# Performance work log

Hardware: AMD Instinct MI355X
Metric: run time of the kernel (lower is better)

The kernel has to match this reference:

```python
import jax, jax.numpy as jnp
import numpy as np

N_ATOMS = 768
BOX_L = 30.0
CUTOFF = 5.0


def _cp(a, b, c):
    # numpy equivalent of torch.cartesian_prod for 1-D inputs
    g = np.meshgrid(a, b, c, indexing='ij')
    return np.stack(g, axis=-1).reshape(-1, 3)


def get_shifts_np(box, pbc, cutoff):
    # host-side mirror of TorchNeighborList._get_shifts (data-dependent shapes)
    recip = np.linalg.inv(box).T
    inv_len = np.linalg.norm(recip, axis=1)
    nrep = np.where(pbc, np.ceil(cutoff * inv_len).astype(np.int64), 0)
    r1 = np.arange(1, nrep[0] + 1)
    r2 = np.arange(1, nrep[1] + 1)
    r3 = np.arange(1, nrep[2] + 1)
    o = np.zeros(1, dtype=np.int64)
    blocks = [_cp(r1, r2, r3), _cp(r1, r2, o), _cp(r1, r2, -r3),
              _cp(r1, o, r3), _cp(r1, o, o), _cp(r1, o, -r3),
              _cp(r1, -r2, r3), _cp(r1, -r2, o), _cp(r1, -r2, -r3),
              _cp(o, r2, r3), _cp(o, r2, o), _cp(o, r2, -r3), _cp(o, o, r3)]
    return np.concatenate(blocks, axis=0).astype(np.int32)


def setup_inputs() -> dict:
    key = jax.random.key(0)
    positions = jax.random.uniform(key, (N_ATOMS, 3), dtype=jnp.float32) * BOX_L
    box = jnp.eye(3, dtype=jnp.float32) * BOX_L
    shifts = jnp.asarray(get_shifts_np(np.eye(3) * BOX_L, np.array([True, True, True]), CUTOFF))  # (13, 3)
    return {"positions": positions, "box": box, "shifts": shifts, "cutoff": CUTOFF}


def reference(positions, box, shifts, cutoff):
    N = positions.shape[0]
    S = shifts.shape[0]
    # central-cell unique pairs i<j (torch.combinations)
    iu, ju = jnp.triu_indices(N, k=1)
    # shifted candidates: cartesian_prod(shift_index, i, j)
    shift_idx = jnp.repeat(jnp.arange(S), N * N)
    pi_s = jnp.tile(jnp.repeat(jnp.arange(N), N), S)
    pj_s = jnp.tile(jnp.arange(N), S * N)
    pi_all = jnp.concatenate([iu, pi_s])          # (P,)
    pj_all = jnp.concatenate([ju, pj_s])          # (P,)
    shifts_all = jnp.concatenate([jnp.zeros((iu.shape[0], 3), dtype=shifts.dtype), shifts[shift_idx]])  # (P,3)
    shift_vals = shifts_all.astype(box.dtype) @ box
    Rij = positions[pi_all] - positions[pj_all] + shift_vals  # (P,3)
    d = jnp.linalg.norm(Rij, axis=1)
    mask = d < cutoff
    # bidirectional pairs (torch.cat of (i,j) and (j,i)), offsets negated for the first half
    bi_i = jnp.concatenate([pi_all, pj_all])
    bi_j = jnp.concatenate([pj_all, pi_all])
    bi_off = jnp.concatenate([-shifts_all, shifts_all])
    bi_mask = jnp.concatenate([mask, mask])
    # jit-compatible compaction: sort by idx_i with invalid entries pushed to the end
    sort_key = jnp.where(bi_mask, bi_i, N)
    order = jnp.argsort(sort_key)  # jax sort is stable
    valid = bi_mask[order]
    idx_i = jnp.where(valid, bi_i[order], -1)
    idx_j = jnp.where(valid, bi_j[order], -1)
    offset = (bi_off[order].astype(box.dtype) @ box) * valid[:, None].astype(box.dtype)
    return idx_i, idx_j, offset, valid
```

## Files before the change

### kernel.cpp

```cpp
#include <hip/hip_runtime.h>

#pragma clang fp contract(off)


#define MAX_SHIFTS 64
#define FILL_ITERS 16

typedef float f32x4 __attribute__((ext_vector_type(4)));

__device__ __forceinline__ bool pv_fwd(float fx, float fy, float fz,
                                       const float* __restrict__ pos, int j,
                                       float sx, float sy, float sz, float cutoff) {
  float dx = fx - pos[j * 3 + 0] + sx;
  float dy = fy - pos[j * 3 + 1] + sy;
  float dz = fz - pos[j * 3 + 2] + sz;
  float d2 = dx * dx + dy * dy + dz * dz;
  return sqrtf(d2) < cutoff;
}

__device__ __forceinline__ bool pv_bwd(const float* __restrict__ pos, int a,
                                       float fx, float fy, float fz,
                                       float sx, float sy, float sz, float cutoff) {
  float dx = pos[a * 3 + 0] - fx + sx;
  float dy = pos[a * 3 + 1] - fy + sy;
  float dz = pos[a * 3 + 2] - fz + sz;
  float d2 = dx * dx + dy * dy + dz * dz;
  return sqrtf(d2) < cutoff;
}

__device__ __forceinline__ void load_shift_vecs(const float* __restrict__ box,
                                                const int* __restrict__ shifts,
                                                int S, float* sv, int tid, int nthreads) {
  for (int s = tid; s < S; s += nthreads) {
    float s0 = (float)shifts[s * 3 + 0];
    float s1 = (float)shifts[s * 3 + 1];
    float s2 = (float)shifts[s * 3 + 2];
    sv[s * 3 + 0] = s0 * box[0] + s1 * box[3] + s2 * box[6];
    sv[s * 3 + 1] = s0 * box[1] + s1 * box[4] + s2 * box[7];
    sv[s * 3 + 2] = s0 * box[2] + s1 * box[5] + s2 * box[8];
  }
}

__device__ __forceinline__ bool axis_ok(float lo, float hi, float cutpad) {
  return (hi > -cutpad) && (lo < cutpad);
}

__global__ __launch_bounds__(256) void k_count(
    const float* __restrict__ pos, const float* __restrict__ box,
    const int* __restrict__ shifts, const float* __restrict__ cutp,
    int N, int S, int* __restrict__ count) {
  __shared__ float sv[MAX_SHIFTS * 3];
  __shared__ float bred[4][6];
  __shared__ int rf[4], rb[4];
  int atom = blockIdx.x;
  int t = threadIdx.x;
  float cut = cutp[0];
  float cutpad = cut + fmaxf(cut * 1e-5f, 1e-5f);
  load_shift_vecs(box, shifts, S, sv, t, blockDim.x);

  float mnx = 1e30f, mny = 1e30f, mnz = 1e30f, mxx = -1e30f, mxy = -1e30f, mxz = -1e30f;
  for (int i = t; i < N; i += blockDim.x) {
    float x = pos[3 * i + 0], y = pos[3 * i + 1], z = pos[3 * i + 2];
    mnx = fminf(mnx, x); mny = fminf(mny, y); mnz = fminf(mnz, z);
    mxx = fmaxf(mxx, x); mxy = fmaxf(mxy, y); mxz = fmaxf(mxz, z);
  }
  for (int off = 32; off; off >>= 1) {
    mnx = fminf(mnx, __shfl_xor(mnx, off)); mny = fminf(mny, __shfl_xor(mny, off));
    mnz = fminf(mnz, __shfl_xor(mnz, off)); mxx = fmaxf(mxx, __shfl_xor(mxx, off));
    mxy = fmaxf(mxy, __shfl_xor(mxy, off)); mxz = fmaxf(mxz, __shfl_xor(mxz, off));
  }
  int w = t >> 6;
  if ((t & 63) == 0) {
    bred[w][0] = mnx; bred[w][1] = mny; bred[w][2] = mnz;
    bred[w][3] = mxx; bred[w][4] = mxy; bred[w][5] = mxz;
  }
  __syncthreads();
  int nw = blockDim.x >> 6;
  mnx = bred[0][0]; mny = bred[0][1]; mnz = bred[0][2];
  mxx = bred[0][3]; mxy = bred[0][4]; mxz = bred[0][5];
  for (int ww = 1; ww < nw; ww++) {
    mnx = fminf(mnx, bred[ww][0]); mny = fminf(mny, bred[ww][1]); mnz = fminf(mnz, bred[ww][2]);
    mxx = fmaxf(mxx, bred[ww][3]); mxy = fmaxf(mxy, bred[ww][4]); mxz = fmaxf(mxz, bred[ww][5]);
  }

  float pix = pos[3 * atom + 0], piy = pos[3 * atom + 1], piz = pos[3 * atom + 2];
  int cf = 0, cb = 0;
  for (int j = atom + 1 + t; j < N; j += blockDim.x)
    if (pv_fwd(pix, piy, piz, pos, j, 0.f, 0.f, 0.f, cut)) cf++;
  for (int a = t; a < atom; a += blockDim.x)
    if (pv_bwd(pos, a, pix, piy, piz, 0.f, 0.f, 0.f, cut)) cb++;

  for (int s = 0; s < S; s++) {
    float svx = sv[3 * s + 0], svy = sv[3 * s + 1], svz = sv[3 * s + 2];
    bool af = axis_ok((pix - mxx) + svx, (pix - mnx) + svx, cutpad) &&
              axis_ok((piy - mxy) + svy, (piy - mny) + svy, cutpad) &&
              axis_ok((piz - mxz) + svz, (piz - mnz) + svz, cutpad);
    if (af) {
      for (int j = t; j < N; j += blockDim.x)
        if (pv_fwd(pix, piy, piz, pos, j, svx, svy, svz, cut)) cf++;
    }
    bool ab = axis_ok((mnx - pix) + svx, (mxx - pix) + svx, cutpad) &&
              axis_ok((mny - piy) + svy, (mxy - piy) + svy, cutpad) &&
              axis_ok((mnz - piz) + svz, (mxz - piz) + svz, cutpad);
    if (ab) {
      for (int a = t; a < N; a += blockDim.x)
        if (pv_bwd(pos, a, pix, piy, piz, svx, svy, svz, cut)) cb++;
    }
  }
  for (int off = 32; off; off >>= 1) {
    cf += __shfl_down(cf, off);
    cb += __shfl_down(cb, off);
  }
  if ((t & 63) == 0) { rf[w] = cf; rb[w] = cb; }
  __syncthreads();
  if (t == 0) {
    int f = 0, b = 0;
    for (int ww = 0; ww < nw; ww++) { f += rf[ww]; b += rb[ww]; }
    count[2 * atom + 0] = f;
    count[2 * atom + 1] = b;
  }
}

__global__ __launch_bounds__(256) void k_main(
    const float* __restrict__ pos, const float* __restrict__ box,
    const int* __restrict__ shifts, const float* __restrict__ cutp,
    int N, int S, const int* __restrict__ count,
    float* __restrict__ out, long M, long n4, int NWB) {
  __shared__ float sv[MAX_SHIFTS * 3];
  int t = threadIdx.x;
  int lane = t & 63, w = t >> 6;
  int n2 = 2 * N;

  if ((int)blockIdx.x < NWB) {
    float cut = cutp[0];
    float cutpad = cut + fmaxf(cut * 1e-5f, 1e-5f);
    load_shift_vecs(box, shifts, S, sv, t, 256);
    __syncthreads();
    int g = blockIdx.x * 4 + w;
    if (g >= n2) return;
    int atom = g >> 1;
    int dir = g & 1;

    float mnx = 1e30f, mny = 1e30f, mnz = 1e30f, mxx = -1e30f, mxy = -1e30f, mxz = -1e30f;
    for (int i = lane; i < N; i += 64) {
      float x = pos[3 * i + 0], y = pos[3 * i + 1], z = pos[3 * i + 2];
      mnx = fminf(mnx, x); mny = fminf(mny, y); mnz = fminf(mnz, z);
      mxx = fmaxf(mxx, x); mxy = fmaxf(mxy, y); mxz = fmaxf(mxz, z);
    }
    for (int off = 32; off; off >>= 1) {
      mnx = fminf(mnx, __shfl_xor(mnx, off)); mny = fminf(mny, __shfl_xor(mny, off));
      mnz = fminf(mnz, __shfl_xor(mnz, off)); mxx = fmaxf(mxx, __shfl_xor(mxx, off));
      mxy = fmaxf(mxy, __shfl_xor(mxy, off)); mxz = fmaxf(mxz, __shfl_xor(mxz, off));
    }

    int pre = 0;
    for (int i = lane; i < g; i += 64) pre += count[i];
    for (int off = 32; off; off >>= 1) pre += __shfl_xor(pre, off);
    long base = pre;

    float* __restrict__ out_i = out;
    float* __restrict__ out_j = out + M;
    float* __restrict__ out_off = out + 2 * M;
    float* __restrict__ out_v = out + 5 * M;

    float pix = pos[3 * atom + 0], piy = pos[3 * atom + 1], piz = pos[3 * atom + 2];
    float fatom = (float)atom;
    int running = 0;

    {
      int n = (dir == 0) ? (N - 1 - atom) : atom;
      int j0 = (dir == 0) ? (atom + 1) : 0;
      float oz0 = (dir == 0) ? -0.0f : 0.0f;
      for (int c0 = 0; c0 < n; c0 += 64) {
        int c = c0 + lane;
        bool v = false;
        int other = j0 + c;
        if (c < n) {
          v = (dir == 0) ? pv_fwd(pix, piy, piz, pos, other, 0.f, 0.f, 0.f, cut)
                         : pv_bwd(pos, other, pix, piy, piz, 0.f, 0.f, 0.f, cut);
        }
        unsigned long long m = __ballot(v);
        if (v) {
          int rank = __popcll(m & ((1ULL << lane) - 1ULL));
          long row = base + running + rank;
          out_i[row] = fatom;
          out_j[row] = (float)other;
          out_off[row * 3 + 0] = oz0;
          out_off[row * 3 + 1] = oz0;
          out_off[row * 3 + 2] = oz0;
          out_v[row] = 1.0f;
        }
        running += __popcll(m);
      }
    }
    for (int s = 0; s < S; s++) {
      float svx = sv[3 * s + 0], svy = sv[3 * s + 1], svz = sv[3 * s + 2];
      bool active;
      if (dir == 0) {
        active = axis_ok((pix - mxx) + svx, (pix - mnx) + svx, cutpad) &&
                 axis_ok((piy - mxy) + svy, (piy - mny) + svy, cutpad) &&
                 axis_ok((piz - mxz) + svz, (piz - mnz) + svz, cutpad);
      } else {
        active = axis_ok((mnx - pix) + svx, (mxx - pix) + svx, cutpad) &&
                 axis_ok((mny - piy) + svy, (mxy - piy) + svy, cutpad) &&
                 axis_ok((mnz - piz) + svz, (mxz - piz) + svz, cutpad);
      }
      if (!active) continue;
      float ox = (dir == 0) ? -svx : svx;
      float oy = (dir == 0) ? -svy : svy;
      float oz = (dir == 0) ? -svz : svz;
      for (int c0 = 0; c0 < N; c0 += 64) {
        int other = c0 + lane;
        bool v = false;
        if (other < N) {
          v = (dir == 0) ? pv_fwd(pix, piy, piz, pos, other, svx, svy, svz, cut)
                         : pv_bwd(pos, other, pix, piy, piz, svx, svy, svz, cut);
        }
        unsigned long long m = __ballot(v);
        if (v) {
          int rank = __popcll(m & ((1ULL << lane) - 1ULL));
          long row = base + running + rank;
          out_i[row] = fatom;
          out_j[row] = (float)other;
          out_off[row * 3 + 0] = ox;
          out_off[row * 3 + 1] = oy;
          out_off[row * 3 + 2] = oz;
          out_v[row] = 1.0f;
        }
        running += __popcll(m);
      }
    }
  } else {
    int tot = 0;
    for (int i = lane; i < n2; i += 64) tot += count[i];
    for (int off = 32; off; off >>= 1) tot += __shfl_xor(tot, off);
    long total = tot;

    long fb = (long)blockIdx.x - NWB;
    long k_lo = fb * (256L * FILL_ITERS);
    long k_hi = k_lo + 256L * FILL_ITERS;
    if (k_hi > n4) k_hi = n4;
    long e_lo = k_lo << 2, e_hi = k_hi << 2;

    long E0 = total;
    long E1 = M + total;
    long E2 = 2 * M + 3 * total;
    long E3 = 5 * M + total;
    const f32x4 neg = {-1.f, -1.f, -1.f, -1.f};
    const f32x4 zer = {0.f, 0.f, 0.f, 0.f};
    f32x4* __restrict__ out4 = (f32x4*)out;

    int s0 = (e_lo < M) ? 0 : ((e_lo < 2 * M) ? 1 : ((e_lo < 5 * M) ? 2 : 3));
    long eh = e_hi - 1;
    int s1 = (eh < M) ? 0 : ((eh < 2 * M) ? 1 : ((eh < 5 * M) ? 2 : 3));
    long ve0 = (s0 == 0) ? E0 : ((s0 == 1) ? E1 : ((s0 == 2) ? E2 : E3));

    if ((k_hi - k_lo) == 256L * FILL_ITERS && s0 == s1 && e_lo >= ve0) {
      f32x4 val = (s0 < 2) ? neg : zer;
      f32x4* __restrict__ p = out4 + k_lo + t;
#pragma unroll
      for (int it = 0; it < FILL_ITERS; it++) p[(long)it * 256] = val;
    } else {
      for (int it = 0; it < FILL_ITERS; it++) {
        long k = k_lo + (long)it * 256 + t;
        if (k >= n4) break;
        long e = k << 2;
        long ve = (e < M) ? E0 : ((e < 2 * M) ? E1 : ((e < 5 * M) ? E2 : E3));
        if (e + 4 <= ve) continue;
        bool isneg = (e < 2 * M);
        if (e >= ve) {
          out4[k] = isneg ? neg : zer;
        } else {
          float dv = isneg ? -1.f : 0.f;
          for (int q = 0; q < 4; q++)
            if (e + q >= ve) out[e + q] = dv;
        }
      }
    }
  }
}

extern "C" void kernel_launch(void* const* d_in, const int* in_sizes, int n_in,
                              void* d_out, int out_size, void* d_ws, size_t ws_size,
                              hipStream_t stream) {
  const float* pos = (const float*)d_in[0];
  const float* box = (const float*)d_in[1];
  const int* shifts = (const int*)d_in[2];
  const float* cutp = (const float*)d_in[3];
  int N = in_sizes[0] / 3;
  int S = in_sizes[2] / 3;
  long M = (long)out_size / 6;
  float* out = (float*)d_out;

  int* count = (int*)d_ws;

  long n4 = (long)out_size / 4;
  int NWB = (2 * N + 3) / 4;
  int NFB = (int)((n4 + (256L * FILL_ITERS) - 1) / (256L * FILL_ITERS));

  hipLaunchKernelGGL(k_count, dim3(N), dim3(256), 0, stream,
                     pos, box, shifts, cutp, N, S, count);
  hipLaunchKernelGGL(k_main, dim3(NWB + NFB), dim3(256), 0, stream,
                     pos, box, shifts, cutp, N, S, count, out, M, n4, NWB);
}
```

Measured before the change: 94.28 us.

## Fuse count and write kernels into persistent kernel with grid barrier

Merges the counting kernel and the main write/fill kernel into one persistent kernel launched with a fixed grid of 256 blocks. Blocks loop over atoms, then meet at a global atomic barrier, then loop over write groups and fill chunks. This removes one kernel launch and the per-warp recomputation of the bounding box, but adds a memset, a spin-wait barrier, and less parallelism in the count phase (256 blocks instead of N). The barrier depends on every block being resident at the same time, which launch_bounds(256,2) is meant to ensure.

```diff
diff --git a/kernel.cpp b/kernel.cpp
--- a/kernel.cpp
+++ b/kernel.cpp
@@ -5,6 +5,7 @@
 
 #define MAX_SHIFTS 64
 #define FILL_ITERS 16
+#define NBLK 256
 
 typedef float f32x4 __attribute__((ext_vector_type(4)));
 
@@ -28,10 +29,25 @@
   return sqrtf(d2) < cutoff;
 }
 
-__device__ __forceinline__ void load_shift_vecs(const float* __restrict__ box,
-                                                const int* __restrict__ shifts,
-                                                int S, float* sv, int tid, int nthreads) {
-  for (int s = tid; s < S; s += nthreads) {
+__device__ __forceinline__ bool axis_ok(float lo, float hi, float cutpad) {
+  return (hi > -cutpad) && (lo < cutpad);
+}
+
+__global__ __launch_bounds__(256, 2) void k_fused(
+    const float* __restrict__ pos, const float* __restrict__ box,
+    const int* __restrict__ shifts, const float* __restrict__ cutp,
+    int N, int S, int* bar, int* count,
+    float* __restrict__ out, long M, long n4, int NWB, int C) {
+  __shared__ float sv[MAX_SHIFTS * 3];
+  __shared__ float bred[4][6];
+  __shared__ int rf[4], rb[4];
+  int t = threadIdx.x;
+  int lane = t & 63, w = t >> 6;
+  int n2 = 2 * N;
+  float cut = cutp[0];
+  float cutpad = cut + fmaxf(cut * 1e-5f, 1e-5f);
+
+  for (int s = t; s < S; s += 256) {
     float s0 = (float)shifts[s * 3 + 0];
     float s1 = (float)shifts[s * 3 + 1];
     float s2 = (float)shifts[s * 3 + 2];
@@ -39,27 +55,9 @@
     sv[s * 3 + 1] = s0 * box[1] + s1 * box[4] + s2 * box[7];
     sv[s * 3 + 2] = s0 * box[2] + s1 * box[5] + s2 * box[8];
   }
-}
-
-__device__ __forceinline__ bool axis_ok(float lo, float hi, float cutpad) {
-  return (hi > -cutpad) && (lo < cutpad);
-}
-
-__global__ __launch_bounds__(256) void k_count(
-    const float* __restrict__ pos, const float* __restrict__ box,
-    const int* __restrict__ shifts, const float* __restrict__ cutp,
-    int N, int S, int* __restrict__ count) {
-  __shared__ float sv[MAX_SHIFTS * 3];
-  __shared__ float bred[4][6];
-  __shared__ int rf[4], rb[4];
-  int atom = blockIdx.x;
-  int t = threadIdx.x;
-  float cut = cutp[0];
-  float cutpad = cut + fmaxf(cut * 1e-5f, 1e-5f);
-  load_shift_vecs(box, shifts, S, sv, t, blockDim.x);
 
   float mnx = 1e30f, mny = 1e30f, mnz = 1e30f, mxx = -1e30f, mxy = -1e30f, mxz = -1e30f;
-  for (int i = t; i < N; i += blockDim.x) {
+  for (int i = t; i < N; i += 256) {
     float x = pos[3 * i + 0], y = pos[3 * i + 1], z = pos[3 * i + 2];
     mnx = fminf(mnx, x); mny = fminf(mny, y); mnz = fminf(mnz, z);
     mxx = fmaxf(mxx, x); mxy = fmaxf(mxy, y); mxz = fmaxf(mxz, z);
@@ -69,99 +67,82 @@
     mnz = fminf(mnz, __shfl_xor(mnz, off)); mxx = fmaxf(mxx, __shfl_xor(mxx, off));
     mxy = fmaxf(mxy, __shfl_xor(mxy, off)); mxz = fmaxf(mxz, __shfl_xor(mxz, off));
   }
-  int w = t >> 6;
   if ((t & 63) == 0) {
     bred[w][0] = mnx; bred[w][1] = mny; bred[w][2] = mnz;
     bred[w][3] = mxx; bred[w][4] = mxy; bred[w][5] = mxz;
   }
   __syncthreads();
-  int nw = blockDim.x >> 6;
   mnx = bred[0][0]; mny = bred[0][1]; mnz = bred[0][2];
   mxx = bred[0][3]; mxy = bred[0][4]; mxz = bred[0][5];
-  for (int ww = 1; ww < nw; ww++) {
+  for (int ww = 1; ww < 4; ww++) {
     mnx = fminf(mnx, bred[ww][0]); mny = fminf(mny, bred[ww][1]); mnz = fminf(mnz, bred[ww][2]);
     mxx = fmaxf(mxx, bred[ww][3]); mxy = fmaxf(mxy, bred[ww][4]); mxz = fmaxf(mxz, bred[ww][5]);
   }
 
-  float pix = pos[3 * atom + 0], piy = pos[3 * atom + 1], piz = pos[3 * atom + 2];
-  int cf = 0, cb = 0;
-  for (int j = atom + 1 + t; j < N; j += blockDim.x)
-    if (pv_fwd(pix, piy, piz, pos, j, 0.f, 0.f, 0.f, cut)) cf++;
-  for (int a = t; a < atom; a += blockDim.x)
-    if (pv_bwd(pos, a, pix, piy, piz, 0.f, 0.f, 0.f, cut)) cb++;
-
-  for (int s = 0; s < S; s++) {
-    float svx = sv[3 * s + 0], svy = sv[3 * s + 1], svz = sv[3 * s + 2];
-    bool af = axis_ok((pix - mxx) + svx, (pix - mnx) + svx, cutpad) &&
-              axis_ok((piy - mxy) + svy, (piy - mny) + svy, cutpad) &&
-              axis_ok((piz - mxz) + svz, (piz - mnz) + svz, cutpad);
-    if (af) {
-      for (int j = t; j < N; j += blockDim.x)
-        if (pv_fwd(pix, piy, piz, pos, j, svx, svy, svz, cut)) cf++;
-    }
-    bool ab = axis_ok((mnx - pix) + svx, (mxx - pix) + svx, cutpad) &&
-              axis_ok((mny - piy) + svy, (mxy - piy) + svy, cutpad) &&
-              axis_ok((mnz - piz) + svz, (mxz - piz) + svz, cutpad);
-    if (ab) {
-      for (int a = t; a < N; a += blockDim.x)
-        if (pv_bwd(pos, a, pix, piy, piz, svx, svy, svz, cut)) cb++;
-    }
-  }
-  for (int off = 32; off; off >>= 1) {
-    cf += __shfl_down(cf, off);
-    cb += __shfl_down(cb, off);
-  }
-  if ((t & 63) == 0) { rf[w] = cf; rb[w] = cb; }
+  for (int atom = blockIdx.x; atom < N; atom += gridDim.x) {
+    float pix = pos[3 * atom + 0], piy = pos[3 * atom + 1], piz = pos[3 * atom + 2];
+    int cf = 0, cb = 0;
+    for (int j = atom + 1 + t; j < N; j += 256)
+      if (pv_fwd(pix, piy, piz, pos, j, 0.f, 0.f, 0.f, cut)) cf++;
+    for (int a = t; a < atom; a += 256)
+      if (pv_bwd(pos, a, pix, piy, piz, 0.f, 0.f, 0.f, cut)) cb++;
+
+    for (int s = 0; s < S; s++) {
+      float svx = sv[3 * s + 0], svy = sv[3 * s + 1], svz = sv[3 * s + 2];
+      bool af = axis_ok((pix - mxx) + svx, (pix - mnx) + svx, cutpad) &&
+                axis_ok((piy - mxy) + svy, (piy - mny) + svy, cutpad) &&
+                axis_ok((piz - mxz) + svz, (piz - mnz) + svz, cutpad);
+      if (af) {
+        for (int j = t; j < N; j += 256)
+          if (pv_fwd(pix, piy, piz, pos, j, svx, svy, svz, cut)) cf++;
+      }
+      bool ab = axis_ok((mnx - pix) + svx, (mxx - pix) + svx, cutpad) &&
+                axis_ok((mny - piy) + svy, (mxy - piy) + svy, cutpad) &&
+                axis_ok((mnz - piz) + svz, (mxz - piz) + svz, cutpad);
+      if (ab) {
+        for (int a = t; a < N; a += 256)
+          if (pv_bwd(pos, a, pix, piy, piz, svx, svy, svz, cut)) cb++;
+      }
+    }
+    for (int off = 32; off; off >>= 1) {
+      cf += __shfl_down(cf, off);
+      cb += __shfl_down(cb, off);
+    }
+    if ((t & 63) == 0) { rf[w] = cf; rb[w] = cb; }
+    __syncthreads();
+    if (t == 0) {
+      count[2 * atom + 0] = rf[0] + rf[1] + rf[2] + rf[3];
+      count[2 * atom + 1] = rb[0] + rb[1] + rb[2] + rb[3];
+    }
+    __syncthreads();
+  }
+
   __syncthreads();
   if (t == 0) {
-    int f = 0, b = 0;
-    for (int ww = 0; ww < nw; ww++) { f += rf[ww]; b += rb[ww]; }
-    count[2 * atom + 0] = f;
-    count[2 * atom + 1] = b;
-  }
-}
-
-__global__ __launch_bounds__(256) void k_main(
-    const float* __restrict__ pos, const float* __restrict__ box,
-    const int* __restrict__ shifts, const float* __restrict__ cutp,
-    int N, int S, const int* __restrict__ count,
-    float* __restrict__ out, long M, long n4, int NWB) {
-  __shared__ float sv[MAX_SHIFTS * 3];
-  int t = threadIdx.x;
-  int lane = t & 63, w = t >> 6;
-  int n2 = 2 * N;
-
-  if ((int)blockIdx.x < NWB) {
-    float cut = cutp[0];
-    float cutpad = cut + fmaxf(cut * 1e-5f, 1e-5f);
-    load_shift_vecs(box, shifts, S, sv, t, 256);
-    __syncthreads();
-    int g = blockIdx.x * 4 + w;
-    if (g >= n2) return;
+    __hip_atomic_fetch_add(bar, 1, __ATOMIC_ACQ_REL, __HIP_MEMORY_SCOPE_AGENT);
+    while (__hip_atomic_load(bar, __ATOMIC_ACQUIRE, __HIP_MEMORY_SCOPE_AGENT) <
+           (int)gridDim.x) {
+      __builtin_amdgcn_s_sleep(2);
+    }
+  }
+  __syncthreads();
+
+  float* __restrict__ out_i = out;
+  float* __restrict__ out_j = out + M;
+  float* __restrict__ out_off = out + 2 * M;
+  float* __restrict__ out_v = out + 5 * M;
+
+  for (int wb = blockIdx.x; wb < NWB; wb += gridDim.x) {
+    int g = wb * 4 + w;
+    if (g >= n2) continue;
     int atom = g >> 1;
     int dir = g & 1;
 
-    float mnx = 1e30f, mny = 1e30f, mnz = 1e30f, mxx = -1e30f, mxy = -1e30f, mxz = -1e30f;
-    for (int i = lane; i < N; i += 64) {
-      float x = pos[3 * i + 0], y = pos[3 * i + 1], z = pos[3 * i + 2];
-      mnx = fminf(mnx, x); mny = fminf(mny, y); mnz = fminf(mnz, z);
-      mxx = fmaxf(mxx, x); mxy = fmaxf(mxy, y); mxz = fmaxf(mxz, z);
-    }
-    for (int off = 32; off; off >>= 1) {
-      mnx = fminf(mnx, __shfl_xor(mnx, off)); mny = fminf(mny, __shfl_xor(mny, off));
-      mnz = fminf(mnz, __shfl_xor(mnz, off)); mxx = fmaxf(mxx, __shfl_xor(mxx, off));
-      mxy = fmaxf(mxy, __shfl_xor(mxy, off)); mxz = fmaxf(mxz, __shfl_xor(mxz, off));
-    }
-
     int pre = 0;
-    for (int i = lane; i < g; i += 64) pre += count[i];
+    for (int i = lane; i < g; i += 64)
+      pre += __hip_atomic_load(&count[i], __ATOMIC_RELAXED, __HIP_MEMORY_SCOPE_AGENT);
     for (int off = 32; off; off >>= 1) pre += __shfl_xor(pre, off);
     long base = pre;
-
-    float* __restrict__ out_i = out;
-    float* __restrict__ out_j = out + M;
-    float* __restrict__ out_off = out + 2 * M;
-    float* __restrict__ out_v = out + 5 * M;
 
     float pix = pos[3 * atom + 0], piy = pos[3 * atom + 1], piz = pos[3 * atom + 2];
     float fatom = (float)atom;
@@ -230,25 +211,27 @@
         running += __popcll(m);
       }
     }
-  } else {
-    int tot = 0;
-    for (int i = lane; i < n2; i += 64) tot += count[i];
-    for (int off = 32; off; off >>= 1) tot += __shfl_xor(tot, off);
-    long total = tot;
-
-    long fb = (long)blockIdx.x - NWB;
-    long k_lo = fb * (256L * FILL_ITERS);
+  }
+
+  int tot = 0;
+  for (int i = lane; i < n2; i += 64)
+    tot += __hip_atomic_load(&count[i], __ATOMIC_RELAXED, __HIP_MEMORY_SCOPE_AGENT);
+  for (int off = 32; off; off >>= 1) tot += __shfl_xor(tot, off);
+  long total = tot;
+
+  long E0 = total;
+  long E1 = M + total;
+  long E2 = 2 * M + 3 * total;
+  long E3 = 5 * M + total;
+  const f32x4 neg = {-1.f, -1.f, -1.f, -1.f};
+  const f32x4 zer = {0.f, 0.f, 0.f, 0.f};
+  f32x4* __restrict__ out4 = (f32x4*)out;
+
+  for (int chunk = blockIdx.x; chunk < C; chunk += gridDim.x) {
+    long k_lo = (long)chunk * (256L * FILL_ITERS);
     long k_hi = k_lo + 256L * FILL_ITERS;
     if (k_hi > n4) k_hi = n4;
     long e_lo = k_lo << 2, e_hi = k_hi << 2;
-
-    long E0 = total;
-    long E1 = M + total;
-    long E2 = 2 * M + 3 * total;
-    long E3 = 5 * M + total;
-    const f32x4 neg = {-1.f, -1.f, -1.f, -1.f};
-    const f32x4 zer = {0.f, 0.f, 0.f, 0.f};
-    f32x4* __restrict__ out4 = (f32x4*)out;
 
     int s0 = (e_lo < M) ? 0 : ((e_lo < 2 * M) ? 1 : ((e_lo < 5 * M) ? 2 : 3));
     long eh = e_hi - 1;
@@ -292,14 +275,15 @@
   long M = (long)out_size / 6;
   float* out = (float*)d_out;
 
-  int* count = (int*)d_ws;
+  int* bar = (int*)d_ws;
+  int* count = (int*)d_ws + 4;
 
   long n4 = (long)out_size / 4;
   int NWB = (2 * N + 3) / 4;
-  int NFB = (int)((n4 + (256L * FILL_ITERS) - 1) / (256L * FILL_ITERS));
-
-  hipLaunchKernelGGL(k_count, dim3(N), dim3(256), 0, stream,
-                     pos, box, shifts, cutp, N, S, count);
-  hipLaunchKernelGGL(k_main, dim3(NWB + NFB), dim3(256), 0, stream,
-                     pos, box, shifts, cutp, N, S, count, out, M, n4, NWB);
-}
+  int C = (int)((n4 + (256L * FILL_ITERS) - 1) / (256L * FILL_ITERS));
+
+  hipMemsetAsync(bar, 0, sizeof(int), stream);
+  hipLaunchKernelGGL(k_fused, dim3(NBLK), dim3(256), 0, stream,
+                     pos, box, shifts, cutp, N, S, bar, count,
+                     out, M, n4, NWB, C);
+}
```

Result: slower. 139.3 us (+47.7%).

## Move padding fill into count kernel, overlapping it with pair counting

Applied to the files above, without the earlier changes.

The full-buffer fill of padding values (-1 for indices, 0 for offsets and valid) moves from the second kernel into the first one. It runs as extra blocks beside the per-atom counting blocks, and the scatter kernel later overwrites the valid rows. The fill no longer has to wait for the counts and skips the per-element boundary logic, so the output write traffic overlaps with counting. The cost is that the whole buffer is written, including rows the scatter then rewrites, which adds some redundant write bandwidth.

```diff
diff --git a/kernel.cpp b/kernel.cpp
--- a/kernel.cpp
+++ b/kernel.cpp
@@ -28,10 +28,47 @@
   return sqrtf(d2) < cutoff;
 }
 
-__device__ __forceinline__ void load_shift_vecs(const float* __restrict__ box,
-                                                const int* __restrict__ shifts,
-                                                int S, float* sv, int tid, int nthreads) {
-  for (int s = tid; s < S; s += nthreads) {
+__device__ __forceinline__ bool axis_ok(float lo, float hi, float cutpad) {
+  return (hi > -cutpad) && (lo < cutpad);
+}
+
+__global__ __launch_bounds__(256) void k_phase1(
+    const float* __restrict__ pos, const float* __restrict__ box,
+    const int* __restrict__ shifts, const float* __restrict__ cutp,
+    int N, int S, int* __restrict__ count,
+    float* __restrict__ out, long M, long n4, int NFB) {
+  int t = threadIdx.x;
+
+  if ((int)blockIdx.x < NFB) {
+    long k_lo = (long)blockIdx.x * (256L * FILL_ITERS);
+    long k_hi = k_lo + 256L * FILL_ITERS;
+    if (k_hi > n4) k_hi = n4;
+    long m4 = (2 * M) >> 2;
+    const f32x4 neg = {-1.f, -1.f, -1.f, -1.f};
+    const f32x4 zer = {0.f, 0.f, 0.f, 0.f};
+    f32x4* __restrict__ out4 = (f32x4*)out;
+
+    if (k_hi - k_lo == 256L * FILL_ITERS && (k_hi <= m4 || k_lo >= m4)) {
+      f32x4 val = (k_lo < m4) ? neg : zer;
+      f32x4* __restrict__ p = out4 + k_lo + t;
+#pragma unroll
+      for (int it = 0; it < FILL_ITERS; it++) p[(long)it * 256] = val;
+    } else {
+      for (long k = k_lo + t; k < k_hi; k += 256)
+        out4[k] = (k < m4) ? neg : zer;
+    }
+    return;
+  }
+
+  __shared__ float sv[MAX_SHIFTS * 3];
+  __shared__ float bred[4][6];
+  __shared__ int rf[4], rb[4];
+  int atom = (int)blockIdx.x - NFB;
+  int w = t >> 6;
+  float cut = cutp[0];
+  float cutpad = cut + fmaxf(cut * 1e-5f, 1e-5f);
+
+  for (int s = t; s < S; s += 256) {
     float s0 = (float)shifts[s * 3 + 0];
     float s1 = (float)shifts[s * 3 + 1];
     float s2 = (float)shifts[s * 3 + 2];
@@ -39,27 +76,9 @@
     sv[s * 3 + 1] = s0 * box[1] + s1 * box[4] + s2 * box[7];
     sv[s * 3 + 2] = s0 * box[2] + s1 * box[5] + s2 * box[8];
   }
-}
-
-__device__ __forceinline__ bool axis_ok(float lo, float hi, float cutpad) {
-  return (hi > -cutpad) && (lo < cutpad);
-}
-
-__global__ __launch_bounds__(256) void k_count(
-    const float* __restrict__ pos, const float* __restrict__ box,
-    const int* __restrict__ shifts, const float* __restrict__ cutp,
-    int N, int S, int* __restrict__ count) {
-  __shared__ float sv[MAX_SHIFTS * 3];
-  __shared__ float bred[4][6];
-  __shared__ int rf[4], rb[4];
-  int atom = blockIdx.x;
-  int t = threadIdx.x;
-  float cut = cutp[0];
-  float cutpad = cut + fmaxf(cut * 1e-5f, 1e-5f);
-  load_shift_vecs(box, shifts, S, sv, t, blockDim.x);
 
   float mnx = 1e30f, mny = 1e30f, mnz = 1e30f, mxx = -1e30f, mxy = -1e30f, mxz = -1e30f;
-  for (int i = t; i < N; i += blockDim.x) {
+  for (int i = t; i < N; i += 256) {
     float x = pos[3 * i + 0], y = pos[3 * i + 1], z = pos[3 * i + 2];
     mnx = fminf(mnx, x); mny = fminf(mny, y); mnz = fminf(mnz, z);
     mxx = fmaxf(mxx, x); mxy = fmaxf(mxy, y); mxz = fmaxf(mxz, z);
@@ -69,25 +88,23 @@
     mnz = fminf(mnz, __shfl_xor(mnz, off)); mxx = fmaxf(mxx, __shfl_xor(mxx, off));
     mxy = fmaxf(mxy, __shfl_xor(mxy, off)); mxz = fmaxf(mxz, __shfl_xor(mxz, off));
   }
-  int w = t >> 6;
   if ((t & 63) == 0) {
     bred[w][0] = mnx; bred[w][1] = mny; bred[w][2] = mnz;
     bred[w][3] = mxx; bred[w][4] = mxy; bred[w][5] = mxz;
   }
   __syncthreads();
-  int nw = blockDim.x >> 6;
   mnx = bred[0][0]; mny = bred[0][1]; mnz = bred[0][2];
   mxx = bred[0][3]; mxy = bred[0][4]; mxz = bred[0][5];
-  for (int ww = 1; ww < nw; ww++) {
+  for (int ww = 1; ww < 4; ww++) {
     mnx = fminf(mnx, bred[ww][0]); mny = fminf(mny, bred[ww][1]); mnz = fminf(mnz, bred[ww][2]);
     mxx = fmaxf(mxx, bred[ww][3]); mxy = fmaxf(mxy, bred[ww][4]); mxz = fmaxf(mxz, bred[ww][5]);
   }
 
   float pix = pos[3 * atom + 0], piy = pos[3 * atom + 1], piz = pos[3 * atom + 2];
   int cf = 0, cb = 0;
-  for (int j = atom + 1 + t; j < N; j += blockDim.x)
+  for (int j = atom + 1 + t; j < N; j += 256)
     if (pv_fwd(pix, piy, piz, pos, j, 0.f, 0.f, 0.f, cut)) cf++;
-  for (int a = t; a < atom; a += blockDim.x)
+  for (int a = t; a < atom; a += 256)
     if (pv_bwd(pos, a, pix, piy, piz, 0.f, 0.f, 0.f, cut)) cb++;
 
   for (int s = 0; s < S; s++) {
@@ -96,14 +113,14 @@
               axis_ok((piy - mxy) + svy, (piy - mny) + svy, cutpad) &&
               axis_ok((piz - mxz) + svz, (piz - mnz) + svz, cutpad);
     if (af) {
-      for (int j = t; j < N; j += blockDim.x)
+      for (int j = t; j < N; j += 256)
         if (pv_fwd(pix, piy, piz, pos, j, svx, svy, svz, cut)) cf++;
     }
     bool ab = axis_ok((mnx - pix) + svx, (mxx - pix) + svx, cutpad) &&
               axis_ok((mny - piy) + svy, (mxy - piy) + svy, cutpad) &&
               axis_ok((mnz - piz) + svz, (mxz - piz) + svz, cutpad);
     if (ab) {
-      for (int a = t; a < N; a += blockDim.x)
+      for (int a = t; a < N; a += 256)
         if (pv_bwd(pos, a, pix, piy, piz, svx, svy, svz, cut)) cb++;
     }
   }
@@ -114,168 +131,125 @@
   if ((t & 63) == 0) { rf[w] = cf; rb[w] = cb; }
   __syncthreads();
   if (t == 0) {
-    int f = 0, b = 0;
-    for (int ww = 0; ww < nw; ww++) { f += rf[ww]; b += rb[ww]; }
-    count[2 * atom + 0] = f;
-    count[2 * atom + 1] = b;
-  }
-}
-
-__global__ __launch_bounds__(256) void k_main(
+    count[2 * atom + 0] = rf[0] + rf[1] + rf[2] + rf[3];
+    count[2 * atom + 1] = rb[0] + rb[1] + rb[2] + rb[3];
+  }
+}
+
+__global__ __launch_bounds__(256) void k_rows(
     const float* __restrict__ pos, const float* __restrict__ box,
     const int* __restrict__ shifts, const float* __restrict__ cutp,
     int N, int S, const int* __restrict__ count,
-    float* __restrict__ out, long M, long n4, int NWB) {
+    float* __restrict__ out, long M) {
   __shared__ float sv[MAX_SHIFTS * 3];
   int t = threadIdx.x;
   int lane = t & 63, w = t >> 6;
   int n2 = 2 * N;
-
-  if ((int)blockIdx.x < NWB) {
-    float cut = cutp[0];
-    float cutpad = cut + fmaxf(cut * 1e-5f, 1e-5f);
-    load_shift_vecs(box, shifts, S, sv, t, 256);
-    __syncthreads();
-    int g = blockIdx.x * 4 + w;
-    if (g >= n2) return;
-    int atom = g >> 1;
-    int dir = g & 1;
-
-    float mnx = 1e30f, mny = 1e30f, mnz = 1e30f, mxx = -1e30f, mxy = -1e30f, mxz = -1e30f;
-    for (int i = lane; i < N; i += 64) {
-      float x = pos[3 * i + 0], y = pos[3 * i + 1], z = pos[3 * i + 2];
-      mnx = fminf(mnx, x); mny = fminf(mny, y); mnz = fminf(mnz, z);
-      mxx = fmaxf(mxx, x); mxy = fmaxf(mxy, y); mxz = fmaxf(mxz, z);
-    }
-    for (int off = 32; off; off >>= 1) {
-      mnx = fminf(mnx, __shfl_xor(mnx, off)); mny = fminf(mny, __shfl_xor(mny, off));
-      mnz = fminf(mnz, __shfl_xor(mnz, off)); mxx = fmaxf(mxx, __shfl_xor(mxx, off));
-      mxy = fmaxf(mxy, __shfl_xor(mxy, off)); mxz = fmaxf(mxz, __shfl_xor(mxz, off));
-    }
-
-    int pre = 0;
-    for (int i = lane; i < g; i += 64) pre += count[i];
-    for (int off = 32; off; off >>= 1) pre += __shfl_xor(pre, off);
-    long base = pre;
-
-    float* __restrict__ out_i = out;
-    float* __restrict__ out_j = out + M;
-    float* __restrict__ out_off = out + 2 * M;
-    float* __restrict__ out_v = out + 5 * M;
-
-    float pix = pos[3 * atom + 0], piy = pos[3 * atom + 1], piz = pos[3 * atom + 2];
-    float fatom = (float)atom;
-    int running = 0;
-
-    {
-      int n = (dir == 0) ? (N - 1 - atom) : atom;
-      int j0 = (dir == 0) ? (atom + 1) : 0;
-      float oz0 = (dir == 0) ? -0.0f : 0.0f;
-      for (int c0 = 0; c0 < n; c0 += 64) {
-        int c = c0 + lane;
-        bool v = false;
-        int other = j0 + c;
-        if (c < n) {
-          v = (dir == 0) ? pv_fwd(pix, piy, piz, pos, other, 0.f, 0.f, 0.f, cut)
-                         : pv_bwd(pos, other, pix, piy, piz, 0.f, 0.f, 0.f, cut);
-        }
-        unsigned long long m = __ballot(v);
-        if (v) {
-          int rank = __popcll(m & ((1ULL << lane) - 1ULL));
-          long row = base + running + rank;
-          out_i[row] = fatom;
-          out_j[row] = (float)other;
-          out_off[row * 3 + 0] = oz0;
-          out_off[row * 3 + 1] = oz0;
-          out_off[row * 3 + 2] = oz0;
-          out_v[row] = 1.0f;
-        }
-        running += __popcll(m);
-      }
-    }
-    for (int s = 0; s < S; s++) {
-      float svx = sv[3 * s + 0], svy = sv[3 * s + 1], svz = sv[3 * s + 2];
-      bool active;
-      if (dir == 0) {
-        active = axis_ok((pix - mxx) + svx, (pix - mnx) + svx, cutpad) &&
-                 axis_ok((piy - mxy) + svy, (piy - mny) + svy, cutpad) &&
-                 axis_ok((piz - mxz) + svz, (piz - mnz) + svz, cutpad);
-      } else {
-        active = axis_ok((mnx - pix) + svx, (mxx - pix) + svx, cutpad) &&
-                 axis_ok((mny - piy) + svy, (mxy - piy) + svy, cutpad) &&
-                 axis_ok((mnz - piz) + svz, (mxz - piz) + svz, cutpad);
-      }
-      if (!active) continue;
-      float ox = (dir == 0) ? -svx : svx;
-      float oy = (dir == 0) ? -svy : svy;
-      float oz = (dir == 0) ? -svz : svz;
-      for (int c0 = 0; c0 < N; c0 += 64) {
-        int other = c0 + lane;
-        bool v = false;
-        if (other < N) {
-          v = (dir == 0) ? pv_fwd(pix, piy, piz, pos, other, svx, svy, svz, cut)
-                         : pv_bwd(pos, other, pix, piy, piz, svx, svy, svz, cut);
-        }
-        unsigned long long m = __ballot(v);
-        if (v) {
-          int rank = __popcll(m & ((1ULL << lane) - 1ULL));
-          long row = base + running + rank;
-          out_i[row] = fatom;
-          out_j[row] = (float)other;
-          out_off[row * 3 + 0] = ox;
-          out_off[row * 3 + 1] = oy;
-          out_off[row * 3 + 2] = oz;
-          out_v[row] = 1.0f;
-        }
-        running += __popcll(m);
-      }
-    }
-  } else {
-    int tot = 0;
-    for (int i = lane; i < n2; i += 64) tot += count[i];
-    for (int off = 32; off; off >>= 1) tot += __shfl_xor(tot, off);
-    long total = tot;
-
-    long fb = (long)blockIdx.x - NWB;
-    long k_lo = fb * (256L * FILL_ITERS);
-    long k_hi = k_lo + 256L * FILL_ITERS;
-    if (k_hi > n4) k_hi = n4;
-    long e_lo = k_lo << 2, e_hi = k_hi << 2;
-
-    long E0 = total;
-    long E1 = M + total;
-    long E2 = 2 * M + 3 * total;
-    long E3 = 5 * M + total;
-    const f32x4 neg = {-1.f, -1.f, -1.f, -1.f};
-    const f32x4 zer = {0.f, 0.f, 0.f, 0.f};
-    f32x4* __restrict__ out4 = (f32x4*)out;
-
-    int s0 = (e_lo < M) ? 0 : ((e_lo < 2 * M) ? 1 : ((e_lo < 5 * M) ? 2 : 3));
-    long eh = e_hi - 1;
-    int s1 = (eh < M) ? 0 : ((eh < 2 * M) ? 1 : ((eh < 5 * M) ? 2 : 3));
-    long ve0 = (s0 == 0) ? E0 : ((s0 == 1) ? E1 : ((s0 == 2) ? E2 : E3));
-
-    if ((k_hi - k_lo) == 256L * FILL_ITERS && s0 == s1 && e_lo >= ve0) {
-      f32x4 val = (s0 < 2) ? neg : zer;
-      f32x4* __restrict__ p = out4 + k_lo + t;
-#pragma unroll
-      for (int it = 0; it < FILL_ITERS; it++) p[(long)it * 256] = val;
+  float cut = cutp[0];
+  float cutpad = cut + fmaxf(cut * 1e-5f, 1e-5f);
+
+  for (int s = t; s < S; s += 256) {
+    float s0 = (float)shifts[s * 3 + 0];
+    float s1 = (float)shifts[s * 3 + 1];
+    float s2 = (float)shifts[s * 3 + 2];
+    sv[s * 3 + 0] = s0 * box[0] + s1 * box[3] + s2 * box[6];
+    sv[s * 3 + 1] = s0 * box[1] + s1 * box[4] + s2 * box[7];
+    sv[s * 3 + 2] = s0 * box[2] + s1 * box[5] + s2 * box[8];
+  }
+  __syncthreads();
+
+  int g = blockIdx.x * 4 + w;
+  if (g >= n2) return;
+  int atom = g >> 1;
+  int dir = g & 1;
+
+  float mnx = 1e30f, mny = 1e30f, mnz = 1e30f, mxx = -1e30f, mxy = -1e30f, mxz = -1e30f;
+  for (int i = lane; i < N; i += 64) {
+    float x = pos[3 * i + 0], y = pos[3 * i + 1], z = pos[3 * i + 2];
+    mnx = fminf(mnx, x); mny = fminf(mny, y); mnz = fminf(mnz, z);
+    mxx = fmaxf(mxx, x); mxy = fmaxf(mxy, y); mxz = fmaxf(mxz, z);
+  }
+  for (int off = 32; off; off >>= 1) {
+    mnx = fminf(mnx, __shfl_xor(mnx, off)); mny = fminf(mny, __shfl_xor(mny, off));
+    mnz = fminf(mnz, __shfl_xor(mnz, off)); mxx = fmaxf(mxx, __shfl_xor(mxx, off));
+    mxy = fmaxf(mxy, __shfl_xor(mxy, off)); mxz = fmaxf(mxz, __shfl_xor(mxz, off));
+  }
+
+  int pre = 0;
+  for (int i = lane; i < g; i += 64) pre += count[i];
+  for (int off = 32; off; off >>= 1) pre += __shfl_xor(pre, off);
+  long base = pre;
+
+  float* __restrict__ out_i = out;
+  float* __restrict__ out_j = out + M;
+  float* __restrict__ out_off = out + 2 * M;
+  float* __restrict__ out_v = out + 5 * M;
+
+  float pix = pos[3 * atom + 0], piy = pos[3 * atom + 1], piz = pos[3 * atom + 2];
+  float fatom = (float)atom;
+  int running = 0;
+
+  {
+    int n = (dir == 0) ? (N - 1 - atom) : atom;
+    int j0 = (dir == 0) ? (atom + 1) : 0;
+    float oz0 = (dir == 0) ? -0.0f : 0.0f;
+    for (int c0 = 0; c0 < n; c0 += 64) {
+      int c = c0 + lane;
+      bool v = false;
+      int other = j0 + c;
+      if (c < n) {
+        v = (dir == 0) ? pv_fwd(pix, piy, piz, pos, other, 0.f, 0.f, 0.f, cut)
+                       : pv_bwd(pos, other, pix, piy, piz, 0.f, 0.f, 0.f, cut);
+      }
+      unsigned long long m = __ballot(v);
+      if (v) {
+        int rank = __popcll(m & ((1ULL << lane) - 1ULL));
+        long row = base + running + rank;
+        out_i[row] = fatom;
+        out_j[row] = (float)other;
+        out_off[row * 3 + 0] = oz0;
+        out_off[row * 3 + 1] = oz0;
+        out_off[row * 3 + 2] = oz0;
+        out_v[row] = 1.0f;
+      }
+      running += __popcll(m);
+    }
+  }
+  for (int s = 0; s < S; s++) {
+    float svx = sv[3 * s + 0], svy = sv[3 * s + 1], svz = sv[3 * s + 2];
+    bool active;
+    if (dir == 0) {
+      active = axis_ok((pix - mxx) + svx, (pix - mnx) + svx, cutpad) &&
+               axis_ok((piy - mxy) + svy, (piy - mny) + svy, cutpad) &&
+               axis_ok((piz - mxz) + svz, (piz - mnz) + svz, cutpad);
     } else {
-      for (int it = 0; it < FILL_ITERS; it++) {
-        long k = k_lo + (long)it * 256 + t;
-        if (k >= n4) break;
-        long e = k << 2;
-        long ve = (e < M) ? E0 : ((e < 2 * M) ? E1 : ((e < 5 * M) ? E2 : E3));
-        if (e + 4 <= ve) continue;
-        bool isneg = (e < 2 * M);
-        if (e >= ve) {
-          out4[k] = isneg ? neg : zer;
-        } else {
-          float dv = isneg ? -1.f : 0.f;
-          for (int q = 0; q < 4; q++)
-            if (e + q >= ve) out[e + q] = dv;
-        }
-      }
+      active = axis_ok((mnx - pix) + svx, (mxx - pix) + svx, cutpad) &&
+               axis_ok((mny - piy) + svy, (mxy - piy) + svy, cutpad) &&
+               axis_ok((mnz - piz) + svz, (mxz - piz) + svz, cutpad);
+    }
+    if (!active) continue;
+    float ox = (dir == 0) ? -svx : svx;
+    float oy = (dir == 0) ? -svy : svy;
+    float oz = (dir == 0) ? -svz : svz;
+    for (int c0 = 0; c0 < N; c0 += 64) {
+      int other = c0 + lane;
+      bool v = false;
+      if (other < N) {
+        v = (dir == 0) ? pv_fwd(pix, piy, piz, pos, other, svx, svy, svz, cut)
+                       : pv_bwd(pos, other, pix, piy, piz, svx, svy, svz, cut);
+      }
+      unsigned long long m = __ballot(v);
+      if (v) {
+        int rank = __popcll(m & ((1ULL << lane) - 1ULL));
+        long row = base + running + rank;
+        out_i[row] = fatom;
+        out_j[row] = (float)other;
+        out_off[row * 3 + 0] = ox;
+        out_off[row * 3 + 1] = oy;
+        out_off[row * 3 + 2] = oz;
+        out_v[row] = 1.0f;
+      }
+      running += __popcll(m);
     }
   }
 }
@@ -295,11 +269,11 @@
   int* count = (int*)d_ws;
 
   long n4 = (long)out_size / 4;
+  int NFB = (int)((n4 + (256L * FILL_ITERS) - 1) / (256L * FILL_ITERS));
   int NWB = (2 * N + 3) / 4;
-  int NFB = (int)((n4 + (256L * FILL_ITERS) - 1) / (256L * FILL_ITERS));
-
-  hipLaunchKernelGGL(k_count, dim3(N), dim3(256), 0, stream,
-                     pos, box, shifts, cutp, N, S, count);
-  hipLaunchKernelGGL(k_main, dim3(NWB + NFB), dim3(256), 0, stream,
-                     pos, box, shifts, cutp, N, S, count, out, M, n4, NWB);
-}
+
+  hipLaunchKernelGGL(k_phase1, dim3(NFB + N), dim3(256), 0, stream,
+                     pos, box, shifts, cutp, N, S, count, out, M, n4, NFB);
+  hipLaunchKernelGGL(k_rows, dim3(NWB), dim3(256), 0, stream,
+                     pos, box, shifts, cutp, N, S, count, out, M);
+}
```

New measurement: 112.0 us. 1.19x slower.
